# Kernel tuning notes

Hardware: AMD Instinct MI355X
Metric: run time of the kernel (lower is better)

## Reference

```python
import jax, jax.numpy as jnp
import numpy as np

ATTN_DIM = 256


def setup_inputs() -> dict:
    key = jax.random.key(0)
    ks = jax.random.split(key, 10)
    B, Cu, Cj, H, W = 4, 320, 1024, 64, 64
    return {
        "unet_feat": jax.random.normal(ks[0], (B, Cu, H, W), jnp.float32),
        "janus_feat": jax.random.normal(ks[1], (B, Cj, H, W), jnp.float32),
        "Wq": jax.random.normal(ks[2], (ATTN_DIM, Cu), jnp.float32) * 0.02,
        "bq": jnp.zeros((ATTN_DIM,), jnp.float32),
        "Wk": jax.random.normal(ks[3], (ATTN_DIM, Cj), jnp.float32) * 0.02,
        "bk": jnp.zeros((ATTN_DIM,), jnp.float32),
        "Wv": jax.random.normal(ks[4], (Cu, Cj), jnp.float32) * 0.02,
        "bv": jnp.zeros((Cu,), jnp.float32),
        "Wo": jax.random.normal(ks[5], (Cu, Cu), jnp.float32) * 0.02,
        "bo": jnp.zeros((Cu,), jnp.float32),
    }


def reference(unet_feat, janus_feat, Wq, bq, Wk, bk, Wv, bv, Wo, bo):
    B, Cu, H, W = unet_feat.shape
    scale = ATTN_DIM ** (-0.5)
    # 1x1 convs == channel matmuls
    q = jnp.einsum('oc,bchw->bohw', Wq, unet_feat) + bq[None, :, None, None]
    k = jnp.einsum('oc,bchw->bohw', Wk, janus_feat) + bk[None, :, None, None]
    v = jnp.einsum('oc,bchw->bohw', Wv, janus_feat) + bv[None, :, None, None]
    N = H * W
    q = q.reshape(B, ATTN_DIM, N).transpose(0, 2, 1)  # [B, N, C]
    k = k.reshape(B, ATTN_DIM, N)                     # [B, C, N]
    v = v.reshape(B, Cu, N)                           # [B, Cu, N]
    attn = jax.nn.softmax(jnp.einsum('bic,bcj->bij', q, k) * scale, axis=-1)
    out = jnp.einsum('bcj,bij->bci', v, attn)         # [B, Cu, N]
    out = out.reshape(B, Cu, H, W)
    out = jnp.einsum('oc,bchw->bohw', Wo, out) + bo[None, :, None, None]
    return unet_feat + out
```

## Files before the change

### kernel.cpp

```cpp
#include <hip/hip_runtime.h>
#include <hip/hip_bf16.h>
#include <math.h>


typedef unsigned short u16;
typedef __attribute__((ext_vector_type(8))) short bf16x8;
typedef __attribute__((ext_vector_type(4))) float f32x4;
typedef __attribute__((ext_vector_type(16))) float f32x16;
typedef __attribute__((ext_vector_type(4))) unsigned short u16x4;

#define NB 4
#define CU 320
#define CJ 1024
#define NN 4096
#define AD 256

#define XU_OFF 0u
#define XJ_OFF 10485760u
#define QB_OFF 44040192u
#define KB_OFF 52428800u
#define VB_OFF 60817408u
#define WQ_OFF 71303168u
#define WK_OFF 71467008u
#define WV_OFF 71991296u
#define WO_OFF 72646656u
#define AO_OFF XU_OFF

__device__ __forceinline__ u16 f2b(float f) {
    union { float f; unsigned u; } v; v.f = f;
    unsigned u = v.u;
    unsigned r = (u + 0x7fffu + ((u >> 16) & 1u)) >> 16;
    return (u16)r;
}

__device__ __forceinline__ float b2f(u16 x) {
    union { unsigned u; float f; } v; v.u = ((unsigned)x) << 16;
    return v.f;
}

__device__ __forceinline__ unsigned cvt_pk_bf16(float lo, float hi) {
    unsigned r;
    asm("v_cvt_pk_bf16_f32 %0, %1, %2" : "=v"(r) : "v"(lo), "v"(hi));
    return r;
}

__device__ __forceinline__ float exp2_fast(float x) {
    float r;
    asm("v_exp_f32 %0, %1" : "=v"(r) : "v"(x));
    return r;
}

__device__ __forceinline__ void async_cp16(const u16* g, char* l) {
    __builtin_amdgcn_global_load_lds(
        (const __attribute__((address_space(1))) unsigned int*)g,
        (__attribute__((address_space(3))) unsigned int*)l, 16, 0, 0);
}

__global__ __launch_bounds__(256) void prep_kernel(
        const float* __restrict__ unet, const float* __restrict__ janus,
        const float* __restrict__ Wq, const float* __restrict__ Wk,
        const float* __restrict__ Wv, const float* __restrict__ Wo,
        u16* __restrict__ Xu, u16* __restrict__ Xj,
        u16* __restrict__ wq, u16* __restrict__ wk,
        u16* __restrict__ wv, u16* __restrict__ wo) {
    __shared__ float tile[64][65];
    int bid = blockIdx.x;
    int t = threadIdx.x;

    if (bid < 5376) {
        const float* src;
        u16* dst;
        int C, x, y, z;
        if (bid < 1280) {
            z = bid / 320; int rem = bid % 320; y = rem / 64; x = rem % 64;
            C = CU; src = unet + (size_t)z * CU * NN; dst = Xu + (size_t)z * NN * CU;
        } else {
            int idx = bid - 1280;
            z = idx / 1024; int rem = idx % 1024; y = rem / 64; x = rem % 64;
            C = CJ; src = janus + (size_t)z * CJ * NN; dst = Xj + (size_t)z * NN * CJ;
        }
        int n0 = x * 64, c0 = y * 64;
        int nl = t & 63, cl = t >> 6;
        #pragma unroll
        for (int k = 0; k < 16; ++k) {
            int c = cl + k * 4;
            tile[c][nl] = src[(size_t)(c0 + c) * NN + n0 + nl];
        }
        __syncthreads();
        int cl2 = t & 63, nl2 = t >> 6;
        #pragma unroll
        for (int k = 0; k < 16; ++k) {
            int n = nl2 + k * 4;
            dst[(size_t)(n0 + n) * C + c0 + cl2] = f2b(tile[cl2][n]);
        }
        return;
    }
    int id = (bid - 5376) * 256 + t;
    if (id < 81920) { wq[id] = f2b(Wq[id]); return; }
    id -= 81920;
    if (id < 262144) { wk[id] = f2b(Wk[id]); return; }
    id -= 262144;
    if (id < 327680) { wv[id] = f2b(Wv[id]); return; }
    id -= 327680;
    if (id < 102400) { wo[id] = f2b(Wo[id]); }
}

template <int KD, int NOUT>
__global__ __launch_bounds__(512, 4) void gemm_final_kernel(
        const u16* __restrict__ A, const u16* __restrict__ W,
        const float* __restrict__ bias, float* __restrict__ outp,
        const float* __restrict__ unet) {
    __shared__ __align__(16) char smem[81920];
    const int t = threadIdx.x;
    const int lane = t & 63, wave = t >> 6;
    const int r = lane & 15, h = lane >> 4;
    const int wr = wave >> 1, wc = wave & 1;
    const int m0 = blockIdx.x * 256;
    const int bn0 = blockIdx.y * 64;

    int goffA[4], goffB;
    #pragma unroll
    for (int n = 0; n < 4; ++n) {
        int c = n * 512 + t;
        int row = c >> 3, s = c & 7;
        goffA[n] = (m0 + row) * KD + ((s ^ (row & 7)) << 3);
    }
    {
        int row = t >> 3, s = t & 7;
        goffB = (bn0 + row) * KD + ((s ^ (row & 7)) << 3);
    }
    const unsigned wb = (unsigned)(t & ~63) * 16u;

    #define GSTAGE(BUF, KT) do {                                                  \
        _Pragma("unroll")                                                         \
        for (int n_ = 0; n_ < 4; ++n_)                                            \
            async_cp16(A + goffA[n_] + (KT) * 64,                                 \
                       smem + (BUF) * 40960 + n_ * 8192 + wb);                    \
        async_cp16(W + goffB + (KT) * 64,                                         \
                   smem + (BUF) * 40960 + 32768 + wb);                            \
    } while (0)

    f32x4 acc[4][2];
    #pragma unroll
    for (int fr = 0; fr < 4; ++fr)
        #pragma unroll
        for (int fc = 0; fc < 2; ++fc) acc[fr][fc] = (f32x4)0.0f;

    GSTAGE(0, 0);
    int buf = 0;
    const int KS = KD / 64;
    for (int kt = 0; kt < KS; ++kt) {
        if (kt < KS - 1) {
            GSTAGE(buf ^ 1, kt + 1);
            asm volatile("s_waitcnt vmcnt(5)" ::: "memory");
        } else {
            asm volatile("s_waitcnt vmcnt(0)" ::: "memory");
        }
        __builtin_amdgcn_s_barrier();
        asm volatile("" ::: "memory");
        const char* Ab = smem + buf * 40960;
        const char* Bb = smem + buf * 40960 + 32768;
        #pragma unroll
        for (int kk = 0; kk < 2; ++kk) {
            bf16x8 af[4], bf[2];
            #pragma unroll
            for (int fr = 0; fr < 4; ++fr) {
                int row = wr * 64 + fr * 16 + r;
                af[fr] = *(const bf16x8*)(Ab + row * 128 + (((kk * 4 + h) ^ (row & 7)) << 4));
            }
            #pragma unroll
            for (int fc = 0; fc < 2; ++fc) {
                int rowb = wc * 32 + fc * 16 + r;
                bf[fc] = *(const bf16x8*)(Bb + rowb * 128 + (((kk * 4 + h) ^ (rowb & 7)) << 4));
            }
            #pragma unroll
            for (int fr = 0; fr < 4; ++fr)
                #pragma unroll
                for (int fc = 0; fc < 2; ++fc)
                    acc[fr][fc] = __builtin_amdgcn_mfma_f32_16x16x32_bf16(
                        af[fr], bf[fc], acc[fr][fc], 0, 0, 0);
        }
        asm volatile("" ::: "memory");
        __builtin_amdgcn_s_barrier();
        asm volatile("" ::: "memory");
        buf ^= 1;
    }
    #undef GSTAGE

    const int mw = m0 + wr * 64;
    const int ob0 = bn0 + wc * 32;

    float* tile = (float*)(smem + wave * 8704);
    #pragma unroll
    for (int fc = 0; fc < 2; ++fc)
        #pragma unroll
        for (int fr = 0; fr < 4; ++fr)
            *(f32x4*)(tile + (fc * 16 + r) * 68 + fr * 16 + h * 4) = acc[fr][fc];
    __builtin_amdgcn_s_waitcnt(0);
    int bb = mw >> 12, nb = mw & 4095;
    #pragma unroll
    for (int g = 0; g < 8; ++g) {
        int chunk = g * 64 + lane;
        int row = chunk >> 4, ns = chunk & 15;
        int o = ob0 + row;
        size_t base = (size_t)bb * CU * NN + (size_t)o * NN + nb + ns * 4;
        f32x4 v = *(const f32x4*)(tile + row * 68 + ns * 4);
        f32x4 u = *(const f32x4*)(unet + base);
        float bs = bias[o];
        f32x4 res;
        #pragma unroll
        for (int rr = 0; rr < 4; ++rr) res[rr] = v[rr] + bs + u[rr];
        *(f32x4*)(outp + base) = res;
    }
}

__global__ __launch_bounds__(512, 4) void gemm_qkv_kernel(
        const u16* __restrict__ Xu, const u16* __restrict__ Xj,
        const u16* __restrict__ wq, const u16* __restrict__ wk,
        const u16* __restrict__ wv, const float* __restrict__ bq,
        const float* __restrict__ bk, const float* __restrict__ bv,
        u16* __restrict__ Qb, u16* __restrict__ Kb, u16* __restrict__ Vb) {
    __shared__ __align__(16) char smem[81920];
    const int t = threadIdx.x;
    const int lane = t & 63, wave = t >> 6;
    const int r = lane & 15, h = lane >> 4;
    const int wr = wave >> 1, wc = wave & 1;
    const int m0 = blockIdx.x * 256;

    const int ytile = blockIdx.y;
    int mode, bn0, KD;
    const u16 *A, *W;
    const float* bias;
    float alpha;
    if (ytile < 4) {
        mode = 0; bn0 = ytile * 64; KD = 1024;
        A = Xj; W = wk; bias = bk; alpha = 1.0f;
    } else if (ytile < 9) {
        mode = 1; bn0 = (ytile - 4) * 64; KD = 1024;
        A = Xj; W = wv; bias = bv; alpha = 1.0f;
    } else {
        mode = 2; bn0 = (ytile - 9) * 64; KD = 320;
        A = Xu; W = wq; bias = bq; alpha = 0.0901684411f;
    }

    int goffA[4], goffB;
    #pragma unroll
    for (int n = 0; n < 4; ++n) {
        int c = n * 512 + t;
        int row = c >> 3, s = c & 7;
        goffA[n] = (m0 + row) * KD + ((s ^ (row & 7)) << 3);
    }
    {
        int row = t >> 3, s = t & 7;
        goffB = (bn0 + row) * KD + ((s ^ (row & 7)) << 3);
    }
    const unsigned wb = (unsigned)(t & ~63) * 16u;

    #define GSTAGE(BUF, KT) do {                                                  \
        _Pragma("unroll")                                                         \
        for (int n_ = 0; n_ < 4; ++n_)                                            \
            async_cp16(A + goffA[n_] + (KT) * 64,                                 \
                       smem + (BUF) * 40960 + n_ * 8192 + wb);                    \
        async_cp16(W + goffB + (KT) * 64,                                         \
                   smem + (BUF) * 40960 + 32768 + wb);                            \
    } while (0)

    f32x4 acc[4][2];
    #pragma unroll
    for (int fr = 0; fr < 4; ++fr)
        #pragma unroll
        for (int fc = 0; fc < 2; ++fc) acc[fr][fc] = (f32x4)0.0f;

    GSTAGE(0, 0);
    int buf = 0;
    const int KS = KD / 64;
    for (int kt = 0; kt < KS; ++kt) {
        if (kt < KS - 1) {
            GSTAGE(buf ^ 1, kt + 1);
            asm volatile("s_waitcnt vmcnt(5)" ::: "memory");
        } else {
            asm volatile("s_waitcnt vmcnt(0)" ::: "memory");
        }
        __builtin_amdgcn_s_barrier();
        asm volatile("" ::: "memory");
        const char* Ab = smem + buf * 40960;
        const char* Bb = smem + buf * 40960 + 32768;
        #pragma unroll
        for (int kk = 0; kk < 2; ++kk) {
            bf16x8 af[4], bf[2];
            #pragma unroll
            for (int fr = 0; fr < 4; ++fr) {
                int row = wr * 64 + fr * 16 + r;
                af[fr] = *(const bf16x8*)(Ab + row * 128 + (((kk * 4 + h) ^ (row & 7)) << 4));
            }
            #pragma unroll
            for (int fc = 0; fc < 2; ++fc) {
                int rowb = wc * 32 + fc * 16 + r;
                bf[fc] = *(const bf16x8*)(Bb + rowb * 128 + (((kk * 4 + h) ^ (rowb & 7)) << 4));
            }
            #pragma unroll
            for (int fr = 0; fr < 4; ++fr)
                #pragma unroll
                for (int fc = 0; fc < 2; ++fc)
                    acc[fr][fc] = __builtin_amdgcn_mfma_f32_16x16x32_bf16(
                        af[fr], bf[fc], acc[fr][fc], 0, 0, 0);
        }
        asm volatile("" ::: "memory");
        __builtin_amdgcn_s_barrier();
        asm volatile("" ::: "memory");
        buf ^= 1;
    }
    #undef GSTAGE

    const int mw = m0 + wr * 64;
    const int ob0 = bn0 + wc * 32;

    if (mode != 1) {
        u16* out = (mode == 2) ? Qb : Kb;
        #pragma unroll
        for (int fc = 0; fc < 2; ++fc) {
            int o = ob0 + fc * 16 + r;
            float bs = bias[o];
            #pragma unroll
            for (int fr = 0; fr < 4; ++fr)
                #pragma unroll
                for (int rr = 0; rr < 4; ++rr) {
                    int mrow = mw + fr * 16 + h * 4 + rr;
                    out[(size_t)mrow * AD + o] = f2b((acc[fr][fc][rr] + bs) * alpha);
                }
        }
    } else {
        u16* tile = (u16*)(smem + wave * 4608);
        #pragma unroll
        for (int fc = 0; fc < 2; ++fc) {
            int o = ob0 + fc * 16 + r;
            float bs = bias[o];
            #pragma unroll
            for (int fr = 0; fr < 4; ++fr) {
                u16x4 v4;
                #pragma unroll
                for (int rr = 0; rr < 4; ++rr) v4[rr] = f2b(acc[fr][fc][rr] + bs);
                *(u16x4*)(tile + (fc * 16 + r) * 72 + fr * 16 + h * 4) = v4;
            }
        }
        __builtin_amdgcn_s_waitcnt(0);
        int bb = mw >> 12, nb = mw & 4095;
        #pragma unroll
        for (int g = 0; g < 4; ++g) {
            int chunk = g * 64 + lane;
            int row = chunk >> 3, ns = chunk & 7;
            int ch = ob0 + row;
            int j = nb + ns * 8;
            bf16x8 val = *(const bf16x8*)(tile + row * 72 + ns * 8);
            size_t off = (size_t)bb * CU * NN + (size_t)(ch >> 5) * (NN * 32)
                       + (size_t)(j >> 4) * 512
                       + (size_t)((ch & 31) + ((j >> 3) & 1) * 32) * 8 + (j & 7);
            *(bf16x8*)(Vb + off) = val;
        }
    }
}

__global__ __launch_bounds__(768, 3) void attn_kernel(
        const u16* __restrict__ Q, const u16* __restrict__ K,
        const u16* __restrict__ V, u16* __restrict__ AO) {
    __shared__ __align__(16) char smem[117248];

    const int t = threadIdx.x;
    const int lane = t & 63;
    const int wave = t >> 6;
    const int r = lane & 31, hi = lane >> 5;

    int linear = blockIdx.x;
    int swz = (linear & 7) * 32 + (linear >> 3);
    int b = swz >> 6;
    int i0 = (swz & 63) * 64;

    const u16* Qb = Q + ((size_t)b * NN + i0) * AD;
    const u16* Kb = K + (size_t)b * NN * AD;
    const u16* Vb = V + (size_t)b * CU * NN;

    {
        #pragma unroll
        for (int n = 0; n < 5; ++n) {
            int id = n * 768 + t;
            if (id < 4096) {
                int tile = id >> 11;
                int idx = id & 2047;
                int row = idx >> 5, c16 = idx & 31;
                async_cp16(Kb + tile * 16384 + row * 256 + ((c16 ^ (row & 31)) << 3),
                           smem + (unsigned)(n * 768 + (t & ~63)) * 16u);
            }
        }
        if (t < 256) {
            int id = 3840 + t;
            int tile = id >> 11;
            int idx = id & 2047;
            int row = idx >> 5, c16 = idx & 31;
            async_cp16(Kb + tile * 16384 + row * 256 + ((c16 ^ (row & 31)) << 3),
                       smem + (unsigned)(3840 + (t & ~63)) * 16u);
        }
    }
    asm volatile("s_waitcnt vmcnt(0)" ::: "memory");
    __builtin_amdgcn_s_barrier();
    asm volatile("" ::: "memory");

    if (wave < 4) {
        const int iw = wave >> 1;
        const int jw = wave & 1;
        bf16x8 q[16];
        #pragma unroll
        for (int kk = 0; kk < 16; ++kk)
            q[kk] = *(const bf16x8*)(Qb + (size_t)(iw * 32 + r) * AD + kk * 16 + hi * 8);
        float m = -INFINITY, lsum = 0.0f;

        for (int i = 0; i < 64; ++i) {
            if (i) {
                __builtin_amdgcn_s_barrier();
                asm volatile("" ::: "memory");
            }
            const char* Kt = smem + (i % 3) * 32768 + jw * 16384;
            f32x16 sa = (f32x16)0.0f, sb = (f32x16)0.0f;
            __builtin_amdgcn_s_setprio(1);
            #pragma unroll
            for (int kk = 0; kk < 8; ++kk) {
                bf16x8 k0 = *(const bf16x8*)(Kt + r * 512 + (((2 * kk + hi) ^ r) << 4));
                bf16x8 k1 = *(const bf16x8*)(Kt + r * 512 + (((2 * (kk + 8) + hi) ^ r) << 4));
                sa = __builtin_amdgcn_mfma_f32_32x32x16_bf16(k0, q[kk], sa, 0, 0, 0);
                sb = __builtin_amdgcn_mfma_f32_32x32x16_bf16(k1, q[kk + 8], sb, 0, 0, 0);
            }
            __builtin_amdgcn_s_setprio(0);
            f32x16 s = sa + sb;

            float x0 = fmaxf(s[0], s[1]),   x1 = fmaxf(s[2], s[3]);
            float x2 = fmaxf(s[4], s[5]),   x3 = fmaxf(s[6], s[7]);
            float x4 = fmaxf(s[8], s[9]),   x5 = fmaxf(s[10], s[11]);
            float x6 = fmaxf(s[12], s[13]), x7 = fmaxf(s[14], s[15]);
            float pmax = fmaxf(fmaxf(fmaxf(x0, x1), fmaxf(x2, x3)),
                               fmaxf(fmaxf(x4, x5), fmaxf(x6, x7)));
            pmax = fmaxf(pmax, __shfl_xor(pmax, 32));
            char* pb = smem + 98304 + (i & 1) * 8960;
            int fl = __any(pmax > m + 8.0f) ? 1 : 0;
            if (fl) {
                float mn = fmaxf(m, pmax);
                float al = exp2_fast(m - mn);
                m = mn;
                lsum *= al;
                if (lane < 32) *(float*)(pb + 8192 + (iw * 2 + jw) * 128 + r * 4) = al;
            }
            if (lane == 0) *(int*)(pb + 8704 + (iw * 2 + jw) * 4) = fl;
            float p[16];
            #pragma unroll
            for (int e = 0; e < 16; ++e) p[e] = exp2_fast(s[e] - m);
            float y0 = (p[0] + p[1]) + (p[2] + p[3]);
            float y1 = (p[4] + p[5]) + (p[6] + p[7]);
            float y2 = (p[8] + p[9]) + (p[10] + p[11]);
            float y3 = (p[12] + p[13]) + (p[14] + p[15]);
            float ps = (y0 + y1) + (y2 + y3);
            ps += __shfl_xor(ps, 32);
            lsum += ps;

            #pragma unroll
            for (int ks = 0; ks < 2; ++ks) {
                unsigned a0 = cvt_pk_bf16(p[8 * ks + 0], p[8 * ks + 1]);
                unsigned a1 = cvt_pk_bf16(p[8 * ks + 2], p[8 * ks + 3]);
                unsigned b0 = cvt_pk_bf16(p[8 * ks + 4], p[8 * ks + 5]);
                unsigned b1 = cvt_pk_bf16(p[8 * ks + 6], p[8 * ks + 7]);
                asm("v_permlane32_swap_b32 %0, %1" : "+v"(a0), "+v"(b0));
                asm("v_permlane32_swap_b32 %0, %1" : "+v"(a1), "+v"(b1));
                union { unsigned w[4]; bf16x8 v; } u;
                u.w[0] = a0; u.w[1] = a1; u.w[2] = b0; u.w[3] = b1;
                *(bf16x8*)(pb + (iw * 2 + jw) * 2048 + ks * 1024 + lane * 16) = u.v;
            }
            asm volatile("s_waitcnt lgkmcnt(0)" ::: "memory");
            __builtin_amdgcn_sched_barrier(0);
        }
        __builtin_amdgcn_s_barrier();
        asm volatile("" ::: "memory");
        if (lane < 32) {
            *(float*)(smem + 116224 + (iw * 2 + jw) * 128 + r * 4) = m;
            *(float*)(smem + 116224 + 512 + (iw * 2 + jw) * 128 + r * 4) = lsum;
        }
        __syncthreads();
        __syncthreads();
        __syncthreads();
    } else {
        const int pvid = wave - 4;
        const int iw = pvid >> 2;
        const int pj = (pvid >> 1) & 1;
        const int cgh = pvid & 1;
        const int tp = t - 256;

        int goffp[4];
        #pragma unroll
        for (int n = 0; n < 4; ++n) {
            int id = n * 512 + tp;
            int row = (id >> 5) & 63;
            int c16 = id & 31;
            goffp[n] = row * 256 + ((c16 ^ (row & 31)) << 3);
        }
        const unsigned wbp = (unsigned)(tp & ~63) * 16u;

        #define STAGE(BUF, KP) do {                                               \
            _Pragma("unroll")                                                     \
            for (int n_ = 0; n_ < 4; ++n_)                                        \
                async_cp16((KP) + goffp[n_],                                      \
                           smem + (BUF) * 32768 + n_ * 8192 + wbp);               \
        } while (0)

        f32x16 o[5];
        #pragma unroll
        for (int ct = 0; ct < 5; ++ct) o[ct] = (f32x16)0.0f;
        const u16* vb = Vb + (size_t)(cgh * 5) * 131072 + lane * 8;

        #define PV_BODY(TI) do {                                                  \
            const char* pb = smem + 98304 + ((TI) & 1) * 8960;                    \
            int fl = *(volatile const int*)(pb + 8704 + (iw * 2 + pj) * 4);       \
            bf16x8 pf0 = *(const bf16x8*)(pb + (iw * 2 + pj) * 2048 + lane * 16); \
            bf16x8 pf1 = *(const bf16x8*)(pb + (iw * 2 + pj) * 2048 + 1024 +      \
                                          lane * 16);                             \
            bf16x8 vfA[5], vfB[5];                                                \
            _Pragma("unroll")                                                     \
            for (int c = 0; c < 5; ++c)                                           \
                vfA[c] = *(const bf16x8*)(vb + (size_t)c * 131072 +               \
                                          ((TI) * 4 + pj * 2 + 0) * 512);         \
            _Pragma("unroll")                                                     \
            for (int c = 0; c < 5; ++c)                                           \
                vfB[c] = *(const bf16x8*)(vb + (size_t)c * 131072 +               \
                                          ((TI) * 4 + pj * 2 + 1) * 512);         \
            if (fl) {                                                             \
                float alv = *(volatile const float*)(pb + 8192 +                  \
                                (iw * 2 + pj) * 128 + (lane & 31) * 4);           \
                _Pragma("unroll")                                                 \
                for (int ct = 0; ct < 5; ++ct) o[ct] *= alv;                      \
            }                                                                     \
            __builtin_amdgcn_s_setprio(1);                                        \
            _Pragma("unroll")                                                     \
            for (int ct = 0; ct < 5; ++ct)                                        \
                o[ct] = __builtin_amdgcn_mfma_f32_32x32x16_bf16(vfA[ct], pf0,     \
                                                                o[ct], 0, 0, 0); \
            _Pragma("unroll")                                                     \
            for (int ct = 0; ct < 5; ++ct)                                        \
                o[ct] = __builtin_amdgcn_mfma_f32_32x32x16_bf16(vfB[ct], pf1,     \
                                                                o[ct], 0, 0, 0); \
            __builtin_amdgcn_s_setprio(0);                                        \
        } while (0)

        for (int i = 0; i < 64; ++i) {
            if (i) {
                __builtin_amdgcn_s_barrier();
                asm volatile("" ::: "memory");
            }
            if (i >= 1) PV_BODY(i - 1);
            if (i <= 61) {
                STAGE((i + 2) % 3, Kb + (i + 2) * 16384);
                asm volatile("s_waitcnt vmcnt(4)" ::: "memory");
            } else {
                asm volatile("s_waitcnt vmcnt(0)" ::: "memory");
            }
        }
        __builtin_amdgcn_s_barrier();
        asm volatile("" ::: "memory");
        PV_BODY(63);

        __syncthreads();
        float m0 = *(const float*)(smem + 116224 + (iw * 2 + pj) * 128 + r * 4);
        float l0 = *(const float*)(smem + 116224 + 512 + (iw * 2 + pj) * 128 + r * 4);
        float m1 = *(const float*)(smem + 116224 + (iw * 2 + (pj ^ 1)) * 128 + r * 4);
        float l1 = *(const float*)(smem + 116224 + 512 + (iw * 2 + (pj ^ 1)) * 128 + r * 4);
        float M = fmaxf(m0, m1);
        float fsc = exp2_fast(m0 - M);
        float fo = exp2_fast(m1 - M);
        float inv = 1.0f / (l0 * fsc + l1 * fo);

        u16* fb = (u16*)smem;
        if (pj == 1) {
            #pragma unroll
            for (int ct = 0; ct < 5; ++ct)
                #pragma unroll
                for (int e = 0; e < 16; ++e) {
                    int c = cgh * 160 + ct * 32 + (e & 3) + 8 * (e >> 2) + 4 * hi;
                    fb[(iw * 32 + r) * 328 + c] = f2b(o[ct][e] * fsc);
                }
        }
        __syncthreads();
        if (pj == 0) {
            #pragma unroll
            for (int ct = 0; ct < 5; ++ct)
                #pragma unroll
                for (int g = 0; g < 4; ++g) {
                    int cb = cgh * 160 + ct * 32 + 8 * g + 4 * hi;
                    u16* fr = &fb[(iw * 32 + r) * 328 + cb];
                    float v0 = (o[ct][4 * g + 0] * fsc + b2f(fr[0])) * inv;
                    float v1 = (o[ct][4 * g + 1] * fsc + b2f(fr[1])) * inv;
                    float v2 = (o[ct][4 * g + 2] * fsc + b2f(fr[2])) * inv;
                    float v3 = (o[ct][4 * g + 3] * fsc + b2f(fr[3])) * inv;
                    *(unsigned*)(fr) = cvt_pk_bf16(v0, v1);
                    *(unsigned*)(fr + 2) = cvt_pk_bf16(v2, v3);
                }
        }
        __syncthreads();
        #undef PV_BODY
        #undef STAGE
    }

    const u16* ob = (const u16*)smem;
    u16* AOb = AO + ((size_t)b * NN + i0) * CU;
    #pragma unroll
    for (int n = 0; n < 3; ++n) {
        int id = n * 768 + t;
        int row = id / 40, c8 = id % 40;
        bf16x8 val = *(const bf16x8*)(ob + row * 328 + c8 * 8);
        *(bf16x8*)(AOb + (size_t)row * CU + c8 * 8) = val;
    }
    if (t < 256) {
        int id = 2304 + t;
        int row = id / 40, c8 = id % 40;
        bf16x8 val = *(const bf16x8*)(ob + row * 328 + c8 * 8);
        *(bf16x8*)(AOb + (size_t)row * CU + c8 * 8) = val;
    }
}

extern "C" void kernel_launch(void* const* d_in, const int* in_sizes, int n_in,
                              void* d_out, int out_size, void* d_ws, size_t ws_size,
                              hipStream_t stream) {
    const float* unet  = (const float*)d_in[0];
    const float* janus = (const float*)d_in[1];
    const float* Wq = (const float*)d_in[2];
    const float* bq = (const float*)d_in[3];
    const float* Wk = (const float*)d_in[4];
    const float* bk = (const float*)d_in[5];
    const float* Wv = (const float*)d_in[6];
    const float* bv = (const float*)d_in[7];
    const float* Wo = (const float*)d_in[8];
    const float* bo = (const float*)d_in[9];
    float* out = (float*)d_out;

    char* ws = (char*)d_ws;
    u16* Xu  = (u16*)(ws + XU_OFF);
    u16* Xj  = (u16*)(ws + XJ_OFF);
    u16* Qb  = (u16*)(ws + QB_OFF);
    u16* Kb  = (u16*)(ws + KB_OFF);
    u16* Vb  = (u16*)(ws + VB_OFF);
    u16* wq  = (u16*)(ws + WQ_OFF);
    u16* wk  = (u16*)(ws + WK_OFF);
    u16* wv  = (u16*)(ws + WV_OFF);
    u16* wo  = (u16*)(ws + WO_OFF);
    u16* AO  = (u16*)(ws + AO_OFF);

    prep_kernel<<<8400, 256, 0, stream>>>(unet, janus, Wq, Wk, Wv, Wo,
                                          Xu, Xj, wq, wk, wv, wo);

    gemm_qkv_kernel<<<dim3(64, 13), 512, 0, stream>>>(
        Xu, Xj, wq, wk, wv, bq, bk, bv, Qb, Kb, Vb);

    attn_kernel<<<256, 768, 0, stream>>>(Qb, Kb, Vb, AO);

    gemm_final_kernel<320, 320><<<dim3(64, 5), 512, 0, stream>>>(
        AO, wo, bo, out, unet);
}
```

Before: 167.8 us.

## Move softmax from QK waves to PV waves and shift K staging to QK waves

The 4 QK waves now only compute raw S tiles, write them as fp32 to shared memory, and issue the async K-tile prefetch. The PV waves, of which there are twice as many, read the scores and do the online-softmax max, exponentials, row sums, bf16 packing and rescaling themselves before their MFMAs. This rebalances the per-stage work between the two warp-specialized groups so the QK waves stop being the bottleneck. In exchange the shared-memory score buffer doubles in size, raising LDS to about 129 KB, and each PV-wave pair computes the exponentials for the same scores twice (redundant across cgh).

```diff
diff --git a/kernel.cpp b/kernel.cpp
--- a/kernel.cpp
+++ b/kernel.cpp
@@ -363,7 +363,7 @@
 __global__ __launch_bounds__(768, 3) void attn_kernel(
         const u16* __restrict__ Q, const u16* __restrict__ K,
         const u16* __restrict__ V, u16* __restrict__ AO) {
-    __shared__ __align__(16) char smem[117248];
+    __shared__ __align__(16) char smem[132096];
 
     const int t = threadIdx.x;
     const int lane = t & 63;
@@ -411,7 +411,16 @@
         #pragma unroll
         for (int kk = 0; kk < 16; ++kk)
             q[kk] = *(const bf16x8*)(Qb + (size_t)(iw * 32 + r) * AD + kk * 16 + hi * 8);
-        float m = -INFINITY, lsum = 0.0f;
+
+        int goffq[8];
+        #pragma unroll
+        for (int n = 0; n < 8; ++n) {
+            int id = n * 256 + t;
+            int row = (id >> 5) & 63;
+            int c16 = id & 31;
+            goffq[n] = row * 256 + ((c16 ^ (row & 31)) << 3);
+        }
+        const unsigned wbq = (unsigned)(t & ~63) * 16u;
 
         for (int i = 0; i < 64; ++i) {
             if (i) {
@@ -419,67 +428,44 @@
                 asm volatile("" ::: "memory");
             }
             const char* Kt = smem + (i % 3) * 32768 + jw * 16384;
-            f32x16 sa = (f32x16)0.0f, sb = (f32x16)0.0f;
+            f32x16 sa = (f32x16)0.0f, sb2 = (f32x16)0.0f;
             __builtin_amdgcn_s_setprio(1);
             #pragma unroll
             for (int kk = 0; kk < 8; ++kk) {
                 bf16x8 k0 = *(const bf16x8*)(Kt + r * 512 + (((2 * kk + hi) ^ r) << 4));
                 bf16x8 k1 = *(const bf16x8*)(Kt + r * 512 + (((2 * (kk + 8) + hi) ^ r) << 4));
                 sa = __builtin_amdgcn_mfma_f32_32x32x16_bf16(k0, q[kk], sa, 0, 0, 0);
-                sb = __builtin_amdgcn_mfma_f32_32x32x16_bf16(k1, q[kk + 8], sb, 0, 0, 0);
+                sb2 = __builtin_amdgcn_mfma_f32_32x32x16_bf16(k1, q[kk + 8], sb2, 0, 0, 0);
             }
             __builtin_amdgcn_s_setprio(0);
-            f32x16 s = sa + sb;
-
-            float x0 = fmaxf(s[0], s[1]),   x1 = fmaxf(s[2], s[3]);
-            float x2 = fmaxf(s[4], s[5]),   x3 = fmaxf(s[6], s[7]);
-            float x4 = fmaxf(s[8], s[9]),   x5 = fmaxf(s[10], s[11]);
-            float x6 = fmaxf(s[12], s[13]), x7 = fmaxf(s[14], s[15]);
-            float pmax = fmaxf(fmaxf(fmaxf(x0, x1), fmaxf(x2, x3)),
-                               fmaxf(fmaxf(x4, x5), fmaxf(x6, x7)));
-            pmax = fmaxf(pmax, __shfl_xor(pmax, 32));
-            char* pb = smem + 98304 + (i & 1) * 8960;
-            int fl = __any(pmax > m + 8.0f) ? 1 : 0;
-            if (fl) {
-                float mn = fmaxf(m, pmax);
-                float al = exp2_fast(m - mn);
-                m = mn;
-                lsum *= al;
-                if (lane < 32) *(float*)(pb + 8192 + (iw * 2 + jw) * 128 + r * 4) = al;
-            }
-            if (lane == 0) *(int*)(pb + 8704 + (iw * 2 + jw) * 4) = fl;
-            float p[16];
-            #pragma unroll
-            for (int e = 0; e < 16; ++e) p[e] = exp2_fast(s[e] - m);
-            float y0 = (p[0] + p[1]) + (p[2] + p[3]);
-            float y1 = (p[4] + p[5]) + (p[6] + p[7]);
-            float y2 = (p[8] + p[9]) + (p[10] + p[11]);
-            float y3 = (p[12] + p[13]) + (p[14] + p[15]);
-            float ps = (y0 + y1) + (y2 + y3);
-            ps += __shfl_xor(ps, 32);
-            lsum += ps;
-
-            #pragma unroll
-            for (int ks = 0; ks < 2; ++ks) {
-                unsigned a0 = cvt_pk_bf16(p[8 * ks + 0], p[8 * ks + 1]);
-                unsigned a1 = cvt_pk_bf16(p[8 * ks + 2], p[8 * ks + 3]);
-                unsigned b0 = cvt_pk_bf16(p[8 * ks + 4], p[8 * ks + 5]);
-                unsigned b1 = cvt_pk_bf16(p[8 * ks + 6], p[8 * ks + 7]);
-                asm("v_permlane32_swap_b32 %0, %1" : "+v"(a0), "+v"(b0));
-                asm("v_permlane32_swap_b32 %0, %1" : "+v"(a1), "+v"(b1));
-                union { unsigned w[4]; bf16x8 v; } u;
-                u.w[0] = a0; u.w[1] = a1; u.w[2] = b0; u.w[3] = b1;
-                *(bf16x8*)(pb + (iw * 2 + jw) * 2048 + ks * 1024 + lane * 16) = u.v;
+            f32x16 s = sa + sb2;
+
+            char* sp = smem + 98304 + (i & 1) * 16384 + (iw * 2 + jw) * 4096
+                     + lane * 16;
+            f32x4 w0, w1, w2, w3;
+            #pragma unroll
+            for (int e = 0; e < 4; ++e) {
+                w0[e] = s[e]; w1[e] = s[4 + e]; w2[e] = s[8 + e]; w3[e] = s[12 + e];
+            }
+            *(f32x4*)(sp)        = w0;
+            *(f32x4*)(sp + 1024) = w1;
+            *(f32x4*)(sp + 2048) = w2;
+            *(f32x4*)(sp + 3072) = w3;
+
+            if (i <= 61) {
+                #pragma unroll
+                for (int n = 0; n < 8; ++n)
+                    async_cp16(Kb + (i + 2) * 16384 + goffq[n],
+                               smem + ((i + 2) % 3) * 32768 + n * 4096 + wbq);
+                asm volatile("s_waitcnt vmcnt(8)" ::: "memory");
+            } else if (i == 62) {
+                asm volatile("s_waitcnt vmcnt(0)" ::: "memory");
             }
             asm volatile("s_waitcnt lgkmcnt(0)" ::: "memory");
             __builtin_amdgcn_sched_barrier(0);
         }
         __builtin_amdgcn_s_barrier();
         asm volatile("" ::: "memory");
-        if (lane < 32) {
-            *(float*)(smem + 116224 + (iw * 2 + jw) * 128 + r * 4) = m;
-            *(float*)(smem + 116224 + 512 + (iw * 2 + jw) * 128 + r * 4) = lsum;
-        }
         __syncthreads();
         __syncthreads();
         __syncthreads();
@@ -488,36 +474,14 @@
         const int iw = pvid >> 2;
         const int pj = (pvid >> 1) & 1;
         const int cgh = pvid & 1;
-        const int tp = t - 256;
-
-        int goffp[4];
-        #pragma unroll
-        for (int n = 0; n < 4; ++n) {
-            int id = n * 512 + tp;
-            int row = (id >> 5) & 63;
-            int c16 = id & 31;
-            goffp[n] = row * 256 + ((c16 ^ (row & 31)) << 3);
-        }
-        const unsigned wbp = (unsigned)(tp & ~63) * 16u;
-
-        #define STAGE(BUF, KP) do {                                               \
-            _Pragma("unroll")                                                     \
-            for (int n_ = 0; n_ < 4; ++n_)                                        \
-                async_cp16((KP) + goffp[n_],                                      \
-                           smem + (BUF) * 32768 + n_ * 8192 + wbp);               \
-        } while (0)
 
         f32x16 o[5];
         #pragma unroll
         for (int ct = 0; ct < 5; ++ct) o[ct] = (f32x16)0.0f;
+        float m = -INFINITY, lsum = 0.0f;
         const u16* vb = Vb + (size_t)(cgh * 5) * 131072 + lane * 8;
 
         #define PV_BODY(TI) do {                                                  \
-            const char* pb = smem + 98304 + ((TI) & 1) * 8960;                    \
-            int fl = *(volatile const int*)(pb + 8704 + (iw * 2 + pj) * 4);       \
-            bf16x8 pf0 = *(const bf16x8*)(pb + (iw * 2 + pj) * 2048 + lane * 16); \
-            bf16x8 pf1 = *(const bf16x8*)(pb + (iw * 2 + pj) * 2048 + 1024 +      \
-                                          lane * 16);                             \
             bf16x8 vfA[5], vfB[5];                                                \
             _Pragma("unroll")                                                     \
             for (int c = 0; c < 5; ++c)                                           \
@@ -527,20 +491,64 @@
             for (int c = 0; c < 5; ++c)                                           \
                 vfB[c] = *(const bf16x8*)(vb + (size_t)c * 131072 +               \
                                           ((TI) * 4 + pj * 2 + 1) * 512);         \
-            if (fl) {                                                             \
-                float alv = *(volatile const float*)(pb + 8192 +                  \
-                                (iw * 2 + pj) * 128 + (lane & 31) * 4);           \
+            const char* sp = smem + 98304 + ((TI) & 1) * 16384 +                  \
+                             (iw * 2 + pj) * 4096 + lane * 16;                    \
+            f32x4 sq0 = *(const f32x4*)(sp);                                      \
+            f32x4 sq1 = *(const f32x4*)(sp + 1024);                               \
+            f32x4 sq2 = *(const f32x4*)(sp + 2048);                               \
+            f32x4 sq3 = *(const f32x4*)(sp + 3072);                               \
+            float s[16];                                                          \
+            _Pragma("unroll")                                                     \
+            for (int e = 0; e < 4; ++e) {                                         \
+                s[e] = sq0[e]; s[4 + e] = sq1[e];                                 \
+                s[8 + e] = sq2[e]; s[12 + e] = sq3[e];                            \
+            }                                                                     \
+            float x0 = fmaxf(s[0], s[1]),   x1 = fmaxf(s[2], s[3]);               \
+            float x2 = fmaxf(s[4], s[5]),   x3 = fmaxf(s[6], s[7]);               \
+            float x4 = fmaxf(s[8], s[9]),   x5 = fmaxf(s[10], s[11]);             \
+            float x6 = fmaxf(s[12], s[13]), x7 = fmaxf(s[14], s[15]);             \
+            float pmax = fmaxf(fmaxf(fmaxf(x0, x1), fmaxf(x2, x3)),               \
+                               fmaxf(fmaxf(x4, x5), fmaxf(x6, x7)));              \
+            pmax = fmaxf(pmax, __shfl_xor(pmax, 32));                             \
+            if (__any(pmax > m + 8.0f)) {                                         \
+                float mn = fmaxf(m, pmax);                                        \
+                float al = exp2_fast(m - mn);                                     \
+                m = mn;                                                           \
+                lsum *= al;                                                       \
                 _Pragma("unroll")                                                 \
-                for (int ct = 0; ct < 5; ++ct) o[ct] *= alv;                      \
+                for (int ct = 0; ct < 5; ++ct) o[ct] *= al;                       \
+            }                                                                     \
+            float p[16];                                                          \
+            _Pragma("unroll")                                                     \
+            for (int e = 0; e < 16; ++e) p[e] = exp2_fast(s[e] - m);              \
+            float y0 = (p[0] + p[1]) + (p[2] + p[3]);                             \
+            float y1 = (p[4] + p[5]) + (p[6] + p[7]);                             \
+            float y2 = (p[8] + p[9]) + (p[10] + p[11]);                           \
+            float y3 = (p[12] + p[13]) + (p[14] + p[15]);                         \
+            float ps = (y0 + y1) + (y2 + y3);                                     \
+            ps += __shfl_xor(ps, 32);                                             \
+            lsum += ps;                                                           \
+            bf16x8 pf[2];                                                         \
+            _Pragma("unroll")                                                     \
+            for (int ks = 0; ks < 2; ++ks) {                                      \
+                unsigned a0 = cvt_pk_bf16(p[8 * ks + 0], p[8 * ks + 1]);          \
+                unsigned a1 = cvt_pk_bf16(p[8 * ks + 2], p[8 * ks + 3]);          \
+                unsigned b0 = cvt_pk_bf16(p[8 * ks + 4], p[8 * ks + 5]);          \
+                unsigned b1 = cvt_pk_bf16(p[8 * ks + 6], p[8 * ks + 7]);          \
+                asm("v_permlane32_swap_b32 %0, %1" : "+v"(a0), "+v"(b0));         \
+                asm("v_permlane32_swap_b32 %0, %1" : "+v"(a1), "+v"(b1));         \
+                union { unsigned w[4]; bf16x8 v; } u;                             \
+                u.w[0] = a0; u.w[1] = a1; u.w[2] = b0; u.w[3] = b1;               \
+                pf[ks] = u.v;                                                     \
             }                                                                     \
             __builtin_amdgcn_s_setprio(1);                                        \
             _Pragma("unroll")                                                     \
             for (int ct = 0; ct < 5; ++ct)                                        \
-                o[ct] = __builtin_amdgcn_mfma_f32_32x32x16_bf16(vfA[ct], pf0,     \
+                o[ct] = __builtin_amdgcn_mfma_f32_32x32x16_bf16(vfA[ct], pf[0],   \
                                                                 o[ct], 0, 0, 0); \
             _Pragma("unroll")                                                     \
             for (int ct = 0; ct < 5; ++ct)                                        \
-                o[ct] = __builtin_amdgcn_mfma_f32_32x32x16_bf16(vfB[ct], pf1,     \
+                o[ct] = __builtin_amdgcn_mfma_f32_32x32x16_bf16(vfB[ct], pf[1],   \
                                                                 o[ct], 0, 0, 0); \
             __builtin_amdgcn_s_setprio(0);                                        \
         } while (0)
@@ -551,26 +559,22 @@
                 asm volatile("" ::: "memory");
             }
             if (i >= 1) PV_BODY(i - 1);
-            if (i <= 61) {
-                STAGE((i + 2) % 3, Kb + (i + 2) * 16384);
-                asm volatile("s_waitcnt vmcnt(4)" ::: "memory");
-            } else {
-                asm volatile("s_waitcnt vmcnt(0)" ::: "memory");
-            }
         }
         __builtin_amdgcn_s_barrier();
         asm volatile("" ::: "memory");
         PV_BODY(63);
 
+        if (cgh == 0 && lane < 32) {
+            *(float*)(smem + 131072 + (iw * 2 + pj) * 128 + r * 4) = m;
+            *(float*)(smem + 131072 + 512 + (iw * 2 + pj) * 128 + r * 4) = lsum;
+        }
         __syncthreads();
-        float m0 = *(const float*)(smem + 116224 + (iw * 2 + pj) * 128 + r * 4);
-        float l0 = *(const float*)(smem + 116224 + 512 + (iw * 2 + pj) * 128 + r * 4);
-        float m1 = *(const float*)(smem + 116224 + (iw * 2 + (pj ^ 1)) * 128 + r * 4);
-        float l1 = *(const float*)(smem + 116224 + 512 + (iw * 2 + (pj ^ 1)) * 128 + r * 4);
-        float M = fmaxf(m0, m1);
-        float fsc = exp2_fast(m0 - M);
+        float m1 = *(const float*)(smem + 131072 + (iw * 2 + (pj ^ 1)) * 128 + r * 4);
+        float l1 = *(const float*)(smem + 131072 + 512 + (iw * 2 + (pj ^ 1)) * 128 + r * 4);
+        float M = fmaxf(m, m1);
+        float fsc = exp2_fast(m - M);
         float fo = exp2_fast(m1 - M);
-        float inv = 1.0f / (l0 * fsc + l1 * fo);
+        float inv = 1.0f / (lsum * fsc + l1 * fo);
 
         u16* fb = (u16*)smem;
         if (pj == 1) {
@@ -600,7 +604,6 @@
         }
         __syncthreads();
         #undef PV_BODY
-        #undef STAGE
     }
 
     const u16* ob = (const u16*)smem;
```

New measurement: 173.9 us. 3.6% more time.
